# Kernel optimization log

Hardware: AMD Instinct MI355X
Metric: run time of the kernel (lower is better)

Reference implementation:

```python
import jax, jax.numpy as jnp
import numpy as np

T, B, I, H = 4096, 64, 128, 1024


def setup_inputs() -> dict:
    key = jax.random.key(0)
    k1, k2, k3, k4, k5 = jax.random.split(key, 5)
    # scale recurrent/input weights so tanh doesn't saturate (ESN-style init)
    x = jax.random.normal(k1, (T, B, I), dtype=jnp.float32)
    weight_ih = jax.random.normal(k2, (H, I), dtype=jnp.float32) / np.sqrt(I)
    weight_hh = jax.random.normal(k3, (H, H), dtype=jnp.float32) * (0.9 / np.sqrt(H))
    bias_ih = jax.random.normal(k4, (H,), dtype=jnp.float32) * 0.1
    bias_hh = jax.random.normal(k5, (H,), dtype=jnp.float32) * 0.1
    return {"x": x, "weight_ih": weight_ih, "weight_hh": weight_hh,
            "bias_ih": bias_ih, "bias_hh": bias_hh}


def reference(x, weight_ih, weight_hh, bias_ih, bias_hh):
    # ESN recurrence: h_t = tanh(x_t @ Wih^T + b_ih + h_{t-1} @ Whh^T + b_hh)
    # x: [T, B, I]; returns final hidden state hx: [B, H]
    def step(h, xt):
        pre = xt @ weight_ih.T + bias_ih + h @ weight_hh.T + bias_hh
        h_new = jnp.tanh(pre)
        return h_new, None

    h0 = jnp.zeros((x.shape[1], weight_hh.shape[0]), dtype=x.dtype)
    h_final, _ = jax.lax.scan(step, h0, x)
    return h_final
```

## Files before the change

### kernel.cpp

```cpp
#include <hip/hip_runtime.h>


#define TT 4096
#define BB 64
#define II 128
#define HH 1024

typedef _Float16 f16x8 __attribute__((ext_vector_type(8)));
typedef float f32x4 __attribute__((ext_vector_type(4)));
typedef unsigned int u32x4 __attribute__((ext_vector_type(4)));

static __device__ __forceinline__ unsigned short f2h_bits(float f) {
    _Float16 h = (_Float16)f;
    return __builtin_bit_cast(unsigned short, h);
}

static __device__ __forceinline__ u32x4 gload16_sc1(const unsigned int* p) {
    u32x4 r;
    asm volatile("global_load_dwordx4 %0, %1, off sc1"
                 : "=v"(r) : "v"(p) : "memory");
    return r;
}

__global__ __launch_bounds__(256, 1) void esn_kernel(
    const float* __restrict__ x, const float* __restrict__ wih,
    const float* __restrict__ whh, const float* __restrict__ bih,
    const float* __restrict__ bhh, float* __restrict__ out,
    unsigned int* __restrict__ hbu0, unsigned int* __restrict__ hbu1,
    unsigned int* __restrict__ flags)
{
    __shared__ __align__(16) unsigned short h_lds[128 * 16 * 8];
    __shared__ __align__(16) unsigned short x_lds[16 * 136];
    __shared__ __align__(16) unsigned int   c_lds[16 * 36];

    const int tid  = threadIdx.x;
    const int lane = tid & 63;
    const int wv   = tid >> 6;
    const int col  = lane & 15;
    const int quad = lane >> 4;

    const int blk    = blockIdx.x;
    const int m      = blk >> 4;
    const int m_base = m * 16;
    const int jj     = blk & 15;
    const int n_idx  = jj * 4 + wv;
    const int n_base = n_idx * 16;

    f16x8 wh[32], wi[4];
#pragma unroll
    for (int kt = 0; kt < 32; ++kt) {
        const float* p = whh + (size_t)(n_base + col) * HH + kt * 32 + quad * 8;
        f16x8 w;
#pragma unroll
        for (int j = 0; j < 8; ++j) w[j] = (_Float16)p[j];
        wh[kt] = w;
    }
#pragma unroll
    for (int kt = 0; kt < 4; ++kt) {
        const float* p = wih + (size_t)(n_base + col) * II + kt * 32 + quad * 8;
        f16x8 w;
#pragma unroll
        for (int j = 0; j < 8; ++j) w[j] = (_Float16)p[j];
        wi[kt] = w;
    }
    const float bias_sum = bih[n_base + col] + bhh[n_base + col];

    const int sr   = tid >> 4;
    const int sc   = tid & 15;
    const int csrc = tid >> 4;
    const int crow = tid & 15;
    const unsigned int* fl = flags + m * 512;

    f32x4 xa, xb;
    {
        const float* gp = x + (size_t)(m_base + sr) * II + sc * 8;
        xa = *(const f32x4*)gp;
        xb = *(const f32x4*)(gp + 4);
    }

    for (int t = 0; t < TT; ++t) {
        const unsigned int* rbu = (t & 1) ? hbu1 : hbu0;
        unsigned int*       wbu = (t & 1) ? hbu0 : hbu1;

        {
            f16x8 v;
#pragma unroll
            for (int j = 0; j < 4; ++j) v[j] = (_Float16)xa[j];
#pragma unroll
            for (int j = 0; j < 4; ++j) v[4 + j] = (_Float16)xb[j];
            *(f16x8*)(x_lds + sr * 136 + sc * 8) = v;
        }

        if (wv == 0) {
            const bool skip = (lane >= 16);
            const unsigned int* fp = fl + lane * 32;
            for (;;) {
                unsigned int v = 0;
                if (!skip)
                    asm volatile("global_load_dword %0, %1, off sc1\n\t"
                                 "s_waitcnt vmcnt(0)"
                                 : "=v"(v) : "v"(fp) : "memory");
                if (__ballot(skip || v >= (unsigned int)t) == ~0ull) break;
            }
        }
        __syncthreads();

        {
            const unsigned int* gp = rbu + (size_t)(m * 16 + csrc) * 512 + crow * 32;
            u32x4 a0 = gload16_sc1(gp);
            u32x4 a1 = gload16_sc1(gp + 4);
            u32x4 a2 = gload16_sc1(gp + 8);
            u32x4 a3 = gload16_sc1(gp + 12);
            u32x4 a4 = gload16_sc1(gp + 16);
            u32x4 a5 = gload16_sc1(gp + 20);
            u32x4 a6 = gload16_sc1(gp + 24);
            u32x4 a7 = gload16_sc1(gp + 28);
            asm volatile("s_waitcnt vmcnt(0)"
                         : "+v"(a0), "+v"(a1), "+v"(a2), "+v"(a3),
                           "+v"(a4), "+v"(a5), "+v"(a6), "+v"(a7)
                         :: "memory");
            unsigned short* lp = h_lds + crow * 8;
            *(u32x4*)(lp + (csrc * 8 + 0) * 128) = a0;
            *(u32x4*)(lp + (csrc * 8 + 1) * 128) = a1;
            *(u32x4*)(lp + (csrc * 8 + 2) * 128) = a2;
            *(u32x4*)(lp + (csrc * 8 + 3) * 128) = a3;
            *(u32x4*)(lp + (csrc * 8 + 4) * 128) = a4;
            *(u32x4*)(lp + (csrc * 8 + 5) * 128) = a5;
            *(u32x4*)(lp + (csrc * 8 + 6) * 128) = a6;
            *(u32x4*)(lp + (csrc * 8 + 7) * 128) = a7;
        }
        __syncthreads();

        if (t + 1 < TT) {
            const float* gp = x + (size_t)(t + 1) * (BB * II)
                              + (size_t)(m_base + sr) * II + sc * 8;
            xa = *(const f32x4*)gp;
            xb = *(const f32x4*)(gp + 4);
        }

        f32x4 acc[4];
#pragma unroll
        for (int i = 0; i < 4; ++i) acc[i] = (f32x4){0.f, 0.f, 0.f, 0.f};
#pragma unroll
        for (int kt = 0; kt < 32; ++kt) {
            f16x8 a = *(const f16x8*)(h_lds + (4 * kt + quad) * 128 + col * 8);
            acc[kt & 3] = __builtin_amdgcn_mfma_f32_16x16x32_f16(
                a, wh[kt], acc[kt & 3], 0, 0, 0);
        }
        const unsigned short* xrow = x_lds + col * 136;
#pragma unroll
        for (int kt = 0; kt < 4; ++kt) {
            f16x8 a = *(const f16x8*)(xrow + kt * 32 + quad * 8);
            acc[kt & 3] = __builtin_amdgcn_mfma_f32_16x16x32_f16(
                a, wi[kt], acc[kt & 3], 0, 0, 0);
        }

        float th[4];
#pragma unroll
        for (int i = 0; i < 4; ++i) {
            float pre = (acc[0][i] + acc[1][i]) + (acc[2][i] + acc[3][i])
                        + bias_sum;
            float pc  = fminf(fmaxf(pre, -9.f), 9.f);
            float e   = __expf(2.f * pc);
            th[i] = (e - 1.f) / (e + 1.f);
        }
        {
            unsigned int p01 = (unsigned int)f2h_bits(th[0]) |
                               ((unsigned int)f2h_bits(th[1]) << 16);
            unsigned int p23 = (unsigned int)f2h_bits(th[2]) |
                               ((unsigned int)f2h_bits(th[3]) << 16);
            unsigned int q01 = (unsigned int)__shfl_xor((int)p01, 1, 64);
            unsigned int q23 = (unsigned int)__shfl_xor((int)p23, 1, 64);
            if (!(lane & 1)) {
                unsigned int w0 = (p01 & 0xFFFFu) | (q01 << 16);
                unsigned int w1 = (p01 >> 16) | (q01 & 0xFFFF0000u);
                unsigned int w2 = (p23 & 0xFFFFu) | (q23 << 16);
                unsigned int w3 = (p23 >> 16) | (q23 & 0xFFFF0000u);
                const int c = wv * 8 + (col >> 1);
                unsigned int* cl = c_lds + (quad * 4) * 36 + c;
                cl[0]      = w0;
                cl[36]     = w1;
                cl[2 * 36] = w2;
                cl[3 * 36] = w3;
            }
        }
        if (t == TT - 1) {
#pragma unroll
            for (int i = 0; i < 4; ++i)
                out[(size_t)(m_base + quad * 4 + i) * HH + n_base + col] = th[i];
        }
        __syncthreads();

        if (t < TT - 1) {
            const int r  = tid >> 4;
            const int c0 = (tid & 15) * 2;
            unsigned int* dst = wbu + (size_t)(m * 16 + jj) * 512 + r * 32 + c0;
            atomicExch(dst,     c_lds[r * 36 + c0]);
            atomicExch(dst + 1, c_lds[r * 36 + c0 + 1]);
            asm volatile("s_waitcnt vmcnt(0)" ::: "memory");
            __syncthreads();
            if (tid == 0)
                atomicExch((unsigned int*)(flags + (m * 16 + jj) * 32),
                           (unsigned int)(t + 1));
        }
    }
}

extern "C" void kernel_launch(void* const* d_in, const int* in_sizes, int n_in,
                              void* d_out, int out_size, void* d_ws, size_t ws_size,
                              hipStream_t stream) {
    const float* x   = (const float*)d_in[0];
    const float* wih = (const float*)d_in[1];
    const float* whh = (const float*)d_in[2];
    const float* bih = (const float*)d_in[3];
    const float* bhh = (const float*)d_in[4];
    float* out = (float*)d_out;

    unsigned int* hbu0  = (unsigned int*)d_ws;
    unsigned int* hbu1  = hbu0 + 32768;
    unsigned int* flags = (unsigned int*)((char*)d_ws + 262144);

    hipMemsetAsync(d_ws, 0, 262144 + 8192, stream);

    esn_kernel<<<dim3(64), dim3(256), 0, stream>>>(x, wih, whh, bih, bhh,
                                                   out, hbu0, hbu1, flags);
}
```

Baseline: 15.45 ms.

## Use 16 blocks of 1024 threads to cut cross-block flag synchronisation

Each block now owns 16 waves covering a quarter of the hidden columns for one batch tile, so each batch tile spans 4 blocks instead of 16. The per-step spin-wait now polls 4 flags instead of 16, each block publishes four h chunks under one flag, and each thread gathers a quarter of the previous h slice into LDS. Block-wide __syncthreads across 1024 threads costs more, and only 16 CUs run, each with 16 waves holding large weight register arrays.

```diff
diff --git a/kernel.cpp b/kernel.cpp
--- a/kernel.cpp
+++ b/kernel.cpp
@@ -22,7 +22,7 @@
     return r;
 }
 
-__global__ __launch_bounds__(256, 1) void esn_kernel(
+__global__ __launch_bounds__(1024, 1) void esn_kernel(
     const float* __restrict__ x, const float* __restrict__ wih,
     const float* __restrict__ whh, const float* __restrict__ bih,
     const float* __restrict__ bhh, float* __restrict__ out,
@@ -31,7 +31,7 @@
 {
     __shared__ __align__(16) unsigned short h_lds[128 * 16 * 8];
     __shared__ __align__(16) unsigned short x_lds[16 * 136];
-    __shared__ __align__(16) unsigned int   c_lds[16 * 36];
+    __shared__ __align__(16) unsigned int   c_lds[16 * 132];
 
     const int tid  = threadIdx.x;
     const int lane = tid & 63;
@@ -40,10 +40,10 @@
     const int quad = lane >> 4;
 
     const int blk    = blockIdx.x;
-    const int m      = blk >> 4;
+    const int m      = blk >> 2;
     const int m_base = m * 16;
-    const int jj     = blk & 15;
-    const int n_idx  = jj * 4 + wv;
+    const int q      = blk & 3;
+    const int n_idx  = q * 16 + wv;
     const int n_base = n_idx * 16;
 
     f16x8 wh[32], wi[4];
@@ -65,14 +65,15 @@
     }
     const float bias_sum = bih[n_base + col] + bhh[n_base + col];
 
-    const int sr   = tid >> 4;
-    const int sc   = tid & 15;
-    const int csrc = tid >> 4;
-    const int crow = tid & 15;
-    const unsigned int* fl = flags + m * 512;
+    const int csrc = tid >> 6;
+    const int crow = (tid >> 2) & 15;
+    const int part = tid & 3;
+    const int sr = (tid >> 4) & 15;
+    const int sc = tid & 15;
+    const unsigned int* fl = flags + m * 128;
 
     f32x4 xa, xb;
-    {
+    if (tid < 256) {
         const float* gp = x + (size_t)(m_base + sr) * II + sc * 8;
         xa = *(const f32x4*)gp;
         xb = *(const f32x4*)(gp + 4);
@@ -82,7 +83,7 @@
         const unsigned int* rbu = (t & 1) ? hbu1 : hbu0;
         unsigned int*       wbu = (t & 1) ? hbu0 : hbu1;
 
-        {
+        if (tid < 256) {
             f16x8 v;
 #pragma unroll
             for (int j = 0; j < 4; ++j) v[j] = (_Float16)xa[j];
@@ -92,7 +93,7 @@
         }
 
         if (wv == 0) {
-            const bool skip = (lane >= 16);
+            const bool skip = (lane >= 4);
             const unsigned int* fp = fl + lane * 32;
             for (;;) {
                 unsigned int v = 0;
@@ -106,32 +107,19 @@
         __syncthreads();
 
         {
-            const unsigned int* gp = rbu + (size_t)(m * 16 + csrc) * 512 + crow * 32;
+            const unsigned int* gp = rbu + (size_t)(m * 16 + csrc) * 512
+                                     + crow * 32 + part * 8;
             u32x4 a0 = gload16_sc1(gp);
             u32x4 a1 = gload16_sc1(gp + 4);
-            u32x4 a2 = gload16_sc1(gp + 8);
-            u32x4 a3 = gload16_sc1(gp + 12);
-            u32x4 a4 = gload16_sc1(gp + 16);
-            u32x4 a5 = gload16_sc1(gp + 20);
-            u32x4 a6 = gload16_sc1(gp + 24);
-            u32x4 a7 = gload16_sc1(gp + 28);
             asm volatile("s_waitcnt vmcnt(0)"
-                         : "+v"(a0), "+v"(a1), "+v"(a2), "+v"(a3),
-                           "+v"(a4), "+v"(a5), "+v"(a6), "+v"(a7)
-                         :: "memory");
+                         : "+v"(a0), "+v"(a1) :: "memory");
             unsigned short* lp = h_lds + crow * 8;
-            *(u32x4*)(lp + (csrc * 8 + 0) * 128) = a0;
-            *(u32x4*)(lp + (csrc * 8 + 1) * 128) = a1;
-            *(u32x4*)(lp + (csrc * 8 + 2) * 128) = a2;
-            *(u32x4*)(lp + (csrc * 8 + 3) * 128) = a3;
-            *(u32x4*)(lp + (csrc * 8 + 4) * 128) = a4;
-            *(u32x4*)(lp + (csrc * 8 + 5) * 128) = a5;
-            *(u32x4*)(lp + (csrc * 8 + 6) * 128) = a6;
-            *(u32x4*)(lp + (csrc * 8 + 7) * 128) = a7;
+            *(u32x4*)(lp + (csrc * 8 + part * 2 + 0) * 128) = a0;
+            *(u32x4*)(lp + (csrc * 8 + part * 2 + 1) * 128) = a1;
         }
         __syncthreads();
 
-        if (t + 1 < TT) {
+        if (tid < 256 && t + 1 < TT) {
             const float* gp = x + (size_t)(t + 1) * (BB * II)
                               + (size_t)(m_base + sr) * II + sc * 8;
             xa = *(const f32x4*)gp;
@@ -176,12 +164,12 @@
                 unsigned int w1 = (p01 >> 16) | (q01 & 0xFFFF0000u);
                 unsigned int w2 = (p23 & 0xFFFFu) | (q23 << 16);
                 unsigned int w3 = (p23 >> 16) | (q23 & 0xFFFF0000u);
-                const int c = wv * 8 + (col >> 1);
-                unsigned int* cl = c_lds + (quad * 4) * 36 + c;
-                cl[0]      = w0;
-                cl[36]     = w1;
-                cl[2 * 36] = w2;
-                cl[3 * 36] = w3;
+                const int cc = (wv >> 2) * 32 + (wv & 3) * 8 + (col >> 1);
+                unsigned int* cl = c_lds + (quad * 4) * 132 + cc;
+                cl[0]       = w0;
+                cl[132]     = w1;
+                cl[2 * 132] = w2;
+                cl[3 * 132] = w3;
             }
         }
         if (t == TT - 1) {
@@ -192,15 +180,17 @@
         __syncthreads();
 
         if (t < TT - 1) {
-            const int r  = tid >> 4;
+            const int ch = tid >> 8;
+            const int rt = (tid >> 4) & 15;
             const int c0 = (tid & 15) * 2;
-            unsigned int* dst = wbu + (size_t)(m * 16 + jj) * 512 + r * 32 + c0;
-            atomicExch(dst,     c_lds[r * 36 + c0]);
-            atomicExch(dst + 1, c_lds[r * 36 + c0 + 1]);
+            unsigned int* dst = wbu + (size_t)(m * 16 + q * 4 + ch) * 512
+                                + rt * 32 + c0;
+            atomicExch(dst,     c_lds[rt * 132 + ch * 32 + c0]);
+            atomicExch(dst + 1, c_lds[rt * 132 + ch * 32 + c0 + 1]);
             asm volatile("s_waitcnt vmcnt(0)" ::: "memory");
             __syncthreads();
             if (tid == 0)
-                atomicExch((unsigned int*)(flags + (m * 16 + jj) * 32),
+                atomicExch((unsigned int*)(flags + (m * 4 + q) * 32),
                            (unsigned int)(t + 1));
         }
     }
@@ -220,8 +210,8 @@
     unsigned int* hbu1  = hbu0 + 32768;
     unsigned int* flags = (unsigned int*)((char*)d_ws + 262144);
 
-    hipMemsetAsync(d_ws, 0, 262144 + 8192, stream);
-
-    esn_kernel<<<dim3(64), dim3(256), 0, stream>>>(x, wih, whh, bih, bhh,
-                                                   out, hbu0, hbu1, flags);
-}
+    hipMemsetAsync(d_ws, 0, 262144 + 2048, stream);
+
+    esn_kernel<<<dim3(16), dim3(1024), 0, stream>>>(x, wih, whh, bih, bhh,
+                                                    out, hbu0, hbu1, flags);
+}
```

Result: slower. 39.45 ms (+155.3%).

## Tag hidden-state words with parity bit and drop drain before barrier

Applied to the files above, without the earlier changes.

Embeds a parity tag bit in each packed fp16 hidden-state word so consumers can check the data itself and re-poll until the expected tag appears, instead of trusting a vmcnt drain before the flag write. The producer now writes each pair of words with a single 64-bit atomic exchange and uses a plain s_barrier without waiting for stores to complete, which takes the store latency off the per-step critical path. This trades a possible reload loop and extra bit ops for one fewer memory drain per step. Clearing bit 30 is meant to be lossless because tanh outputs stay below 2 in magnitude, but it relies on the flag still being loosely ordered with the data. A timeout poisons the output if polling never succeeds.

```diff
diff --git a/kernel.cpp b/kernel.cpp
--- a/kernel.cpp
+++ b/kernel.cpp
@@ -5,6 +5,7 @@
 #define BB 64
 #define II 128
 #define HH 1024
+#define TAGBIT 0x40000000u
 
 typedef _Float16 f16x8 __attribute__((ext_vector_type(8)));
 typedef float f32x4 __attribute__((ext_vector_type(4)));
@@ -78,9 +79,13 @@
         xb = *(const f32x4*)(gp + 4);
     }
 
+    unsigned int fail = 0;
     for (int t = 0; t < TT; ++t) {
         const unsigned int* rbu = (t & 1) ? hbu1 : hbu0;
         unsigned int*       wbu = (t & 1) ? hbu0 : hbu1;
+        const unsigned int etag =
+            (t == 0) ? 0u : ((1u ^ (((unsigned)(t - 1) >> 1) & 1u)) << 30);
+        const unsigned int my_tag = (1u ^ (((unsigned)t >> 1) & 1u)) << 30;
 
         {
             f16x8 v;
@@ -115,10 +120,31 @@
             u32x4 a5 = gload16_sc1(gp + 20);
             u32x4 a6 = gload16_sc1(gp + 24);
             u32x4 a7 = gload16_sc1(gp + 28);
-            asm volatile("s_waitcnt vmcnt(0)"
-                         : "+v"(a0), "+v"(a1), "+v"(a2), "+v"(a3),
-                           "+v"(a4), "+v"(a5), "+v"(a6), "+v"(a7)
-                         :: "memory");
+            int rounds = 0;
+            for (;;) {
+                asm volatile("s_waitcnt vmcnt(0)"
+                             : "+v"(a0), "+v"(a1), "+v"(a2), "+v"(a3),
+                               "+v"(a4), "+v"(a5), "+v"(a6), "+v"(a7)
+                             :: "memory");
+                unsigned int bad =
+                    (a0[0] ^ etag) | (a0[2] ^ etag) | (a1[0] ^ etag) | (a1[2] ^ etag) |
+                    (a2[0] ^ etag) | (a2[2] ^ etag) | (a3[0] ^ etag) | (a3[2] ^ etag) |
+                    (a4[0] ^ etag) | (a4[2] ^ etag) | (a5[0] ^ etag) | (a5[2] ^ etag) |
+                    (a6[0] ^ etag) | (a6[2] ^ etag) | (a7[0] ^ etag) | (a7[2] ^ etag);
+                if (!(bad & TAGBIT)) break;
+                if (++rounds > 65536) { fail = 1u; break; }
+                a0 = gload16_sc1(gp);
+                a1 = gload16_sc1(gp + 4);
+                a2 = gload16_sc1(gp + 8);
+                a3 = gload16_sc1(gp + 12);
+                a4 = gload16_sc1(gp + 16);
+                a5 = gload16_sc1(gp + 20);
+                a6 = gload16_sc1(gp + 24);
+                a7 = gload16_sc1(gp + 28);
+            }
+            const unsigned int clr = ~TAGBIT;
+            a0 &= clr; a1 &= clr; a2 &= clr; a3 &= clr;
+            a4 &= clr; a5 &= clr; a6 &= clr; a7 &= clr;
             unsigned short* lp = h_lds + crow * 8;
             *(u32x4*)(lp + (csrc * 8 + 0) * 128) = a0;
             *(u32x4*)(lp + (csrc * 8 + 1) * 128) = a1;
@@ -172,10 +198,10 @@
             unsigned int q01 = (unsigned int)__shfl_xor((int)p01, 1, 64);
             unsigned int q23 = (unsigned int)__shfl_xor((int)p23, 1, 64);
             if (!(lane & 1)) {
-                unsigned int w0 = (p01 & 0xFFFFu) | (q01 << 16);
-                unsigned int w1 = (p01 >> 16) | (q01 & 0xFFFF0000u);
-                unsigned int w2 = (p23 & 0xFFFFu) | (q23 << 16);
-                unsigned int w3 = (p23 >> 16) | (q23 & 0xFFFF0000u);
+                unsigned int w0 = ((p01 & 0xFFFFu) | (q01 << 16)) | my_tag;
+                unsigned int w1 = ((p01 >> 16) | (q01 & 0xFFFF0000u)) | my_tag;
+                unsigned int w2 = ((p23 & 0xFFFFu) | (q23 << 16)) | my_tag;
+                unsigned int w3 = ((p23 >> 16) | (q23 & 0xFFFF0000u)) | my_tag;
                 const int c = wv * 8 + (col >> 1);
                 unsigned int* cl = c_lds + (quad * 4) * 36 + c;
                 cl[0]      = w0;
@@ -187,18 +213,22 @@
         if (t == TT - 1) {
 #pragma unroll
             for (int i = 0; i < 4; ++i)
-                out[(size_t)(m_base + quad * 4 + i) * HH + n_base + col] = th[i];
+                out[(size_t)(m_base + quad * 4 + i) * HH + n_base + col] =
+                    th[i] + (fail ? 1e30f : 0.f);
         }
         __syncthreads();
 
         if (t < TT - 1) {
             const int r  = tid >> 4;
             const int c0 = (tid & 15) * 2;
-            unsigned int* dst = wbu + (size_t)(m * 16 + jj) * 512 + r * 32 + c0;
-            atomicExch(dst,     c_lds[r * 36 + c0]);
-            atomicExch(dst + 1, c_lds[r * 36 + c0 + 1]);
-            asm volatile("s_waitcnt vmcnt(0)" ::: "memory");
-            __syncthreads();
+            unsigned long long vv =
+                (unsigned long long)c_lds[r * 36 + c0] |
+                ((unsigned long long)c_lds[r * 36 + c0 + 1] << 32);
+            atomicExch((unsigned long long*)
+                       (wbu + (size_t)(m * 16 + jj) * 512 + r * 32 + c0), vv);
+            __builtin_amdgcn_sched_barrier(0);
+            __builtin_amdgcn_s_barrier();
+            __builtin_amdgcn_sched_barrier(0);
             if (tid == 0)
                 atomicExch((unsigned int*)(flags + (m * 16 + jj) * 32),
                            (unsigned int)(t + 1));
```

Result: faster. 14.09 ms (-8.8%).
